# Kernel optimization log

Measured on AMD Instinct MI355X. Metric: run time of the kernel, lower is better.

## Reference

```python
import jax, jax.numpy as jnp
import numpy as np
from math import sqrt

IN_DIM = 4096
OUT_DIM = 32
TW = 2            # tree_width (forced to 2 by the forward's pairwise stacking)
TREE_DEPTH = 22
T = TREE_DEPTH - 1  # number of loop iterations (module decrements tree_depth)


def _w(k, out_dim, in_dim):
    # mimics init_weights_unif: U(-1,1)/sqrt(out_dim) + eye (preserve=True default)
    x = (jax.random.uniform(k, (out_dim, in_dim)) * 2 - 1) / sqrt(out_dim)
    return x + jnp.eye(out_dim, in_dim)


def _b(k, dim):
    return (jax.random.uniform(k, (dim,)) * 2 - 1) / sqrt(dim)


def setup_inputs() -> dict:
    key = jax.random.key(0)
    ks = jax.random.split(key, 14)
    return {
        "x": jax.random.normal(ks[0], (IN_DIM,), dtype=jnp.float32),
        "in_left_layer": _w(ks[1], TW, IN_DIM),
        "in_right_layer": _w(ks[2], TW, IN_DIM),
        "in_left_bias": _b(ks[3], TW),
        "in_right_bias": _b(ks[4], TW),
        "tree_left_layers": jnp.stack([_w(k, TW, TW) for k in jax.random.split(ks[5], T)]),
        "tree_right_layers": jnp.stack([_w(k, TW, TW) for k in jax.random.split(ks[6], T)]),
        "tree_left_biases": jnp.stack([_b(k, TW) for k in jax.random.split(ks[7], T)]),
        "tree_right_biases": jnp.stack([_b(k, TW) for k in jax.random.split(ks[8], T)]),
        "out_layer0": _w(ks[9], OUT_DIM, IN_DIM),
        "out_layers": jnp.stack([_w(k, OUT_DIM, TW) for k in jax.random.split(ks[10], T)]),
        "out_bias": _b(ks[11], OUT_DIM),
    }


def reference(x, in_left_layer, in_right_layer, in_left_bias, in_right_bias,
              tree_left_layers, tree_right_layers, tree_left_biases,
              tree_right_biases, out_layer0, out_layers, out_bias):
    # Faithful to BinTreeNetwork.forward: the per-j torch.tensor([li_j, ri_j])
    # construction is exactly jnp.stack([left, right], axis=1); the
    # ComponentNetwork is constructed in __init__ but never used in forward.
    left = x @ in_left_layer.T + in_left_bias      # (TW,)
    right = x @ in_right_layer.T + in_right_bias   # (TW,)
    out = x @ out_layer0.T                          # (OUT_DIM,)
    n_iter = tree_left_layers.shape[0]
    for i in range(n_iter):  # fixed small structural loop; shapes differ per level
        # res: binary-tree expansion, shape (2,)*(i+2); res[j,0]=left[j], res[j,1]=right[j]
        res = jnp.stack([left, right], axis=1)
        left = res @ tree_left_layers[i].T + tree_left_biases[i]
        right = res @ tree_right_layers[i].T + tree_right_biases[i]
        # out broadcasts: (2,)*i+(OUT_DIM,) + (2,)*(i+1)+(OUT_DIM,)
        out = out + res @ out_layers[i].T
    return out + out_bias  # shape (2,)*T + (OUT_DIM,)
```

## Files before the change

kernel.cpp:

```cpp
#include <hip/hip_runtime.h>
#include <hip/hip_bf16.h>


#define P0 (1u << 19)
#define C14OFF (1u << 20)
#define C16OFF (1u << 21)

typedef float floatx4 __attribute__((ext_vector_type(4)));

__global__ __launch_bounds__(1024) void k_dots(
    const float* __restrict__ x,
    const float* __restrict__ inL,
    const float* __restrict__ inR,
    const float* __restrict__ outL0,
    float* __restrict__ ws)
{
    __shared__ float red[16];
    const int d = blockIdx.x;
    const int tid = threadIdx.x;
    const float* row =
        (d < 2) ? inL + d * 4096 :
        (d < 4) ? inR + (d - 2) * 4096 :
                  outL0 + (d - 4) * 4096;
    floatx4 a = ((const floatx4*)row)[tid];
    floatx4 b = ((const floatx4*)x)[tid];
    float s = a.x * b.x + a.y * b.y + a.z * b.z + a.w * b.w;
    #pragma unroll
    for (int off = 32; off; off >>= 1) s += __shfl_down(s, off, 64);
    if ((tid & 63) == 0) red[tid >> 6] = s;
    __syncthreads();
    if (tid < 16) {
        float v = red[tid];
        #pragma unroll
        for (int off = 8; off; off >>= 1) v += __shfl_down(v, off, 16);
        if (tid == 0) ws[P0 + 1664 + d] = v;
    }
}

__global__ __launch_bounds__(256) void k_paths(
    const float* __restrict__ treeL,
    const float* __restrict__ treeR,
    const float* __restrict__ treeLb,
    const float* __restrict__ treeRb,
    const float* __restrict__ inLb,
    const float* __restrict__ inRb,
    float* __restrict__ ws)
{
    const unsigned t = blockIdx.x * 256u + threadIdx.x;
    const float* dots = ws + P0 + 1664;

    if (t < 2) {
        ws[t * 2 + 0] = dots[t]     + inLb[t];
        ws[t * 2 + 1] = dots[2 + t] + inRb[t];
    }
    if (t >= (1u << 18) - 4) return;

    const unsigned u = t + 4u;
    const int i = (31 - __clz(u)) - 1;
    unsigned m = u - (1u << (i + 1));
    unsigned sbits = 0;
    for (int l = i; l >= 1; --l) {
        sbits |= ((m >> (l - 1)) & 1u) << l;
        m = ((m >> l) << (l - 1)) | (m & ((1u << (l - 1)) - 1u));
    }
    float v0 = dots[m]     + inLb[m];
    float v1 = dots[2 + m] + inRb[m];
    for (int l = 1; l <= i; ++l) {
        const int s = (sbits >> l) & 1;
        const float* W  = (s ? treeR  : treeL)  + (l - 1) * 4;
        const float* bb = (s ? treeRb : treeLb) + (l - 1) * 2;
        const float n0 = W[0] * v0 + W[1] * v1 + bb[0];
        const float n1 = W[2] * v0 + W[3] * v1 + bb[1];
        v0 = n0; v1 = n1;
    }
    ws[2 * t + 4] = v0;
    ws[2 * t + 5] = v1;
}

__global__ __launch_bounds__(256) void k_c16f(
    const float* __restrict__ outLs,
    const float* __restrict__ outB,
    float* __restrict__ ws)
{
    const unsigned m = blockIdx.x * 256u + threadIdx.x;
    const float* dots = ws + P0 + 1664;

    float acc[32];
    #pragma unroll
    for (int o = 0; o < 32; ++o) acc[o] = dots[4 + o] + outB[o];
    #pragma unroll
    for (int i = 0; i <= 16; ++i) {
        const float2 v = *(const float2*)(ws + ((1u << (i + 2)) - 4)
                                             + (m & ((2u << i) - 1)) * 2);
        const float* cf = outLs + i * 64;
        #pragma unroll
        for (int o = 0; o < 32; ++o)
            acc[o] += v.x * cf[o * 2] + v.y * cf[o * 2 + 1];
    }
    floatx4* dst = (floatx4*)(ws + C16OFF + (size_t)m * 32);
    #pragma unroll
    for (int q = 0; q < 8; ++q)
        dst[q] = (floatx4){acc[q * 4 + 0], acc[q * 4 + 1],
                           acc[q * 4 + 2], acc[q * 4 + 3]};
}

__global__ __launch_bounds__(256) void k_final_c16(
    const float* __restrict__ ws,
    const float* __restrict__ outLs,
    const float* __restrict__ treeL,
    const float* __restrict__ treeR,
    const float* __restrict__ treeLb,
    const float* __restrict__ treeRb,
    float* __restrict__ out)
{
    __shared__ floatx4 st[256 * 8];
    const int tid = threadIdx.x;
    const unsigned B = blockIdx.x * 256u + tid;
    const float* C16 = ws + C16OFF;

    float acc[32];
    {
        const floatx4* c4 = (const floatx4*)(C16 + (size_t)(B & 0x1FFFFu) * 32);
        #pragma unroll
        for (int q = 0; q < 8; ++q) {
            floatx4 v = c4[q];
            acc[q * 4 + 0] = v.x; acc[q * 4 + 1] = v.y;
            acc[q * 4 + 2] = v.z; acc[q * 4 + 3] = v.w;
        }
    }

    {
        const unsigned Blo = B & 0xFFFFu;
        const float* r16 = ws + ((1u << 18) - 4);
        float2 vA = *(const float2*)(r16 + Blo * 2);
        float2 vC = *(const float2*)(r16 + (Blo + 65536u) * 2);
        float A0 = vA.x, A1 = vA.y;
        float c0 = vC.x, c1 = vC.y;
        #pragma unroll
        for (int l = 17; l <= 20; ++l) {
            const int s = (B >> (l - 1)) & 1;
            const float* WL = treeL  + (l - 1) * 4;
            const float* WR = treeR  + (l - 1) * 4;
            const float* bL = treeLb + (l - 1) * 2;
            const float* bR = treeRb + (l - 1) * 2;
            const float w00 = s ? WR[0] : WL[0], w01 = s ? WR[1] : WL[1];
            const float w10 = s ? WR[2] : WL[2], w11 = s ? WR[3] : WL[3];
            const float b0  = s ? bR[0] : bL[0], b1  = s ? bR[1] : bL[1];
            const float nA0 = w00 * A0 + w01 * A1 + b0;
            const float nA1 = w10 * A0 + w11 * A1 + b1;
            const float nc0 = w00 * c0 + w01 * c1 + b0;
            const float nc1 = w10 * c0 + w11 * c1 + b1;
            A0 = nA0; A1 = nA1; c0 = nc0; c1 = nc1;
            const int pick = (B >> l) & 1;
            const float q0 = pick ? c0 : A0, q1 = pick ? c1 : A1;
            const float* cf = outLs + l * 64;
            #pragma unroll
            for (int o = 0; o < 32; ++o)
                acc[o] += q0 * cf[o * 2] + q1 * cf[o * 2 + 1];
        }
    }

    #pragma unroll
    for (int q = 0; q < 8; ++q) {
        st[tid * 8 + (q ^ (tid & 7))] =
            (floatx4){acc[q * 4 + 0], acc[q * 4 + 1],
                      acc[q * 4 + 2], acc[q * 4 + 3]};
    }
    __syncthreads();
    {
        const int w = tid >> 6, lane = tid & 63;
        const int x = (lane & 7) ^ (lane >> 3);
        floatx4* dst = (floatx4*)(out + (size_t)blockIdx.x * 8192u
                                      + (unsigned)w * 2048u + (unsigned)lane * 4u);
        #pragma unroll
        for (int j = 0; j < 8; ++j) {
            const int m = w * 64 + j * 8 + (lane >> 3);
            __builtin_nontemporal_store(st[m * 8 + x], dst + j * 64);
        }
    }
}

__global__ __launch_bounds__(1024) void k_levels(
    const float* __restrict__ inLb,
    const float* __restrict__ inRb,
    const float* __restrict__ treeL,
    const float* __restrict__ treeR,
    const float* __restrict__ treeLb,
    const float* __restrict__ treeRb,
    const float* __restrict__ outLs,
    const float* __restrict__ outB,
    float* __restrict__ ws)
{
    const int tid = threadIdx.x;
    float* base  = ws + P0;
    float* outLf = ws + P0 + 32;
    float* tLf   = ws + P0 + 1376;
    float* tRf   = ws + P0 + 1460;
    float* tLbf  = ws + P0 + 1544;
    float* tRbf  = ws + P0 + 1586;
    const float* dots = ws + P0 + 1664;
    float* C7    = ws + P0 + 2048;

    for (int i = tid; i < 21 * 64; i += 1024) outLf[i] = outLs[i];
    if (tid < 84)                      tLf[tid]        = treeL[tid];
    else if (tid < 168)                tRf[tid - 84]   = treeR[tid - 84];
    else if (tid < 210)                tLbf[tid - 168] = treeLb[tid - 168];
    else if (tid < 252)                tRbf[tid - 210] = treeRb[tid - 210];
    if (tid < 32) base[tid] = dots[4 + tid] + outB[tid];
    if (tid < 2) {
        ws[tid * 2 + 0] = dots[tid]     + inLb[tid];
        ws[tid * 2 + 1] = dots[2 + tid] + inRb[tid];
    }
    __syncthreads();

    for (int i = 1; i <= 13; ++i) {
        const float* prev = ws + ((1u << (i + 1)) - 4);
        float* cur        = ws + ((1u << (i + 2)) - 4);
        const int rows = 1 << (i + 1);
        const int lowmask = (1 << (i - 1)) - 1;
        for (int m = tid; m < rows; m += 1024) {
            const int src = ((m >> i) << (i - 1)) | (m & lowmask);
            const int s = (m >> (i - 1)) & 1;
            const float* W  = (s ? tRf  : tLf)  + (i - 1) * 4;
            const float* bb = (s ? tRbf : tLbf) + (i - 1) * 2;
            const float p0 = prev[src * 2], p1 = prev[src * 2 + 1];
            cur[m * 2 + 0] = W[0] * p0 + W[1] * p1 + bb[0];
            cur[m * 2 + 1] = W[2] * p0 + W[3] * p1 + bb[1];
        }
        __syncthreads();
    }

    for (int idx = tid; idx < 8192; idx += 1024) {
        const int m = idx >> 5, o = idx & 31;
        float s = base[o];
        #pragma unroll
        for (int i = 0; i < 8; ++i) {
            const float* ri = ws + ((1u << (i + 2)) - 4) + (m & ((2 << i) - 1)) * 2;
            s += ri[0] * outLf[i * 64 + o * 2] + ri[1] * outLf[i * 64 + o * 2 + 1];
        }
        C7[idx] = s;
    }
}

__global__ __launch_bounds__(256) void k_mid(float* __restrict__ ws)
{
    const int blk = blockIdx.x;
    int j, b;
    if      (blk < 16) { j = 14; b = blk; }
    else if (blk < 48) { j = 15; b = blk - 16; }
    else               { j = 16; b = blk - 48; }

    const float* tLf  = ws + P0 + 1376;
    const float* tRf  = ws + P0 + 1460;
    const float* tLbf = ws + P0 + 1544;
    const float* tRbf = ws + P0 + 1586;

    unsigned m = (unsigned)b << 11;
    const unsigned basej = m;
    unsigned sbits = 0;
    for (int l = j; l > 13; --l) {
        sbits |= ((m >> (l - 1)) & 1u) << l;
        m = ((m >> l) << (l - 1)) | (m & ((1u << (l - 1)) - 1));
    }

    const int r0 = threadIdx.x * 8;
    const floatx4* s4 = (const floatx4*)(ws + ((1u << 15) - 4) + (m + r0) * 2);
    floatx4 a0 = s4[0], a1 = s4[1], a2 = s4[2], a3 = s4[3];
    float r[8][2] = {{a0.x,a0.y},{a0.z,a0.w},{a1.x,a1.y},{a1.z,a1.w},
                     {a2.x,a2.y},{a2.z,a2.w},{a3.x,a3.y},{a3.z,a3.w}};

    for (int l = 14; l <= j; ++l) {
        const int s = (sbits >> l) & 1;
        const float* W  = (s ? tRf  : tLf)  + (l - 1) * 4;
        const float* bb = (s ? tRbf : tLbf) + (l - 1) * 2;
        const float w00 = W[0], w01 = W[1], w10 = W[2], w11 = W[3];
        const float b0 = bb[0], b1 = bb[1];
        #pragma unroll
        for (int q = 0; q < 8; ++q) {
            const float p0 = r[q][0], p1 = r[q][1];
            r[q][0] = w00 * p0 + w01 * p1 + b0;
            r[q][1] = w10 * p0 + w11 * p1 + b1;
        }
    }

    floatx4* d4 = (floatx4*)(ws + ((1u << (j + 2)) - 4) + (basej + r0) * 2);
    d4[0] = (floatx4){r[0][0], r[0][1], r[1][0], r[1][1]};
    d4[1] = (floatx4){r[2][0], r[2][1], r[3][0], r[3][1]};
    d4[2] = (floatx4){r[4][0], r[4][1], r[5][0], r[5][1]};
    d4[3] = (floatx4){r[6][0], r[6][1], r[7][0], r[7][1]};
}

__global__ __launch_bounds__(256) void k_c14(float* __restrict__ ws)
{
    const unsigned m = blockIdx.x * 256u + threadIdx.x;
    const float* outLf = ws + P0 + 32;
    const float* C7    = ws + P0 + 2048;

    float acc[32];
    const floatx4* c4 = (const floatx4*)(C7 + (m & 255u) * 32);
    #pragma unroll
    for (int q = 0; q < 8; ++q) {
        floatx4 v = c4[q];
        acc[q * 4 + 0] = v.x; acc[q * 4 + 1] = v.y;
        acc[q * 4 + 2] = v.z; acc[q * 4 + 3] = v.w;
    }
    #pragma unroll
    for (int i = 8; i <= 14; ++i) {
        const float2 v = *(const float2*)(ws + ((1u << (i + 2)) - 4)
                                             + (m & ((2u << i) - 1)) * 2);
        const float* cf = outLf + i * 64;
        #pragma unroll
        for (int o = 0; o < 32; ++o)
            acc[o] += v.x * cf[o * 2] + v.y * cf[o * 2 + 1];
    }
    floatx4* dst = (floatx4*)(ws + C14OFF + m * 32);
    #pragma unroll
    for (int q = 0; q < 8; ++q)
        dst[q] = (floatx4){acc[q * 4 + 0], acc[q * 4 + 1],
                           acc[q * 4 + 2], acc[q * 4 + 3]};
}

__global__ __launch_bounds__(256) void k_final_fold(const float* __restrict__ ws,
                                                    float* __restrict__ out)
{
    __shared__ floatx4 st[256 * 8];
    const int tid = threadIdx.x;
    const unsigned B = blockIdx.x * 256u + tid;
    const float* outLf = ws + P0 + 32;
    const float* tLf   = ws + P0 + 1376;
    const float* tRf   = ws + P0 + 1460;
    const float* tLbf  = ws + P0 + 1544;
    const float* tRbf  = ws + P0 + 1586;
    const float* C14   = ws + C14OFF;

    float acc[32];
    {
        const floatx4* c4 = (const floatx4*)(C14 + (B & 0x7FFFu) * 32);
        #pragma unroll
        for (int q = 0; q < 8; ++q) {
            floatx4 v = c4[q];
            acc[q * 4 + 0] = v.x; acc[q * 4 + 1] = v.y;
            acc[q * 4 + 2] = v.z; acc[q * 4 + 3] = v.w;
        }
    }
    {
        const float2 v = *(const float2*)(ws + ((1u << 17) - 4)
                                             + (B & 0xFFFFu) * 2);
        const float* cf = outLf + 15 * 64;
        #pragma unroll
        for (int o = 0; o < 32; ++o)
            acc[o] += v.x * cf[o * 2] + v.y * cf[o * 2 + 1];
    }
    {
        const unsigned Blo = B & 0xFFFFu;
        const float* r16 = ws + ((1u << 18) - 4);
        float2 vA = *(const float2*)(r16 + Blo * 2);
        float2 vC = *(const float2*)(r16 + (Blo + 65536u) * 2);
        float A0 = vA.x, A1 = vA.y;
        float c0 = vC.x, c1 = vC.y;
        {
            const int pick = (B >> 16) & 1;
            const float q0 = pick ? c0 : A0, q1 = pick ? c1 : A1;
            const float* cf = outLf + 16 * 64;
            #pragma unroll
            for (int o = 0; o < 32; ++o)
                acc[o] += q0 * cf[o * 2] + q1 * cf[o * 2 + 1];
        }
        #pragma unroll
        for (int l = 17; l <= 20; ++l) {
            const int s = (B >> (l - 1)) & 1;
            const float* WL = tLf + (l - 1) * 4;
            const float* WR = tRf + (l - 1) * 4;
            const float* bL = tLbf + (l - 1) * 2;
            const float* bR = tRbf + (l - 1) * 2;
            const float w00 = s ? WR[0] : WL[0], w01 = s ? WR[1] : WL[1];
            const float w10 = s ? WR[2] : WL[2], w11 = s ? WR[3] : WL[3];
            const float b0  = s ? bR[0] : bL[0], b1  = s ? bR[1] : bL[1];
            const float nA0 = w00 * A0 + w01 * A1 + b0;
            const float nA1 = w10 * A0 + w11 * A1 + b1;
            const float nc0 = w00 * c0 + w01 * c1 + b0;
            const float nc1 = w10 * c0 + w11 * c1 + b1;
            A0 = nA0; A1 = nA1; c0 = nc0; c1 = nc1;
            const int pick = (B >> l) & 1;
            const float q0 = pick ? c0 : A0, q1 = pick ? c1 : A1;
            const float* cf = outLf + l * 64;
            #pragma unroll
            for (int o = 0; o < 32; ++o)
                acc[o] += q0 * cf[o * 2] + q1 * cf[o * 2 + 1];
        }
    }
    #pragma unroll
    for (int q = 0; q < 8; ++q) {
        st[tid * 8 + (q ^ (tid & 7))] =
            (floatx4){acc[q * 4 + 0], acc[q * 4 + 1],
                      acc[q * 4 + 2], acc[q * 4 + 3]};
    }
    __syncthreads();
    {
        const int w = tid >> 6, lane = tid & 63;
        const int x = (lane & 7) ^ (lane >> 3);
        floatx4* dst = (floatx4*)(out + (size_t)blockIdx.x * 8192u
                                      + (unsigned)w * 2048u + (unsigned)lane * 4u);
        #pragma unroll
        for (int j = 0; j < 8; ++j) {
            const int m = w * 64 + j * 8 + (lane >> 3);
            __builtin_nontemporal_store(st[m * 8 + x], dst + j * 64);
        }
    }
}

__global__ __launch_bounds__(256) void k_final_legacy(const float* __restrict__ ws,
                                                      float* __restrict__ out)
{
    __shared__ floatx4 st[256 * 8];
    const int tid = threadIdx.x;
    const unsigned B = blockIdx.x * 256u + tid;
    const float* outLf = ws + P0 + 32;
    const float* tLf   = ws + P0 + 1376;
    const float* tRf   = ws + P0 + 1460;
    const float* tLbf  = ws + P0 + 1544;
    const float* tRbf  = ws + P0 + 1586;
    const float* C7    = ws + P0 + 2048;

    float acc[32];
    {
        const floatx4* c4 = (const floatx4*)(C7 + (B & 255u) * 32);
        #pragma unroll
        for (int q = 0; q < 8; ++q) {
            floatx4 v = c4[q];
            acc[q * 4 + 0] = v.x; acc[q * 4 + 1] = v.y;
            acc[q * 4 + 2] = v.z; acc[q * 4 + 3] = v.w;
        }
    }
    float p[8][2];
    #pragma unroll
    for (int i = 8; i <= 15; ++i) {
        const float2* ri = (const float2*)(ws + ((1u << (i + 2)) - 4)
                                              + (B & ((2u << i) - 1)) * 2);
        float2 v = *ri;
        p[i - 8][0] = v.x;
        p[i - 8][1] = v.y;
    }
    #pragma unroll
    for (int i = 0; i < 8; ++i) {
        const float* cf = outLf + (i + 8) * 64;
        const float q0 = p[i][0], q1 = p[i][1];
        #pragma unroll
        for (int o = 0; o < 32; ++o)
            acc[o] += q0 * cf[o * 2] + q1 * cf[o * 2 + 1];
    }
    {
        const unsigned Blo = B & 0xFFFFu;
        const float* r16 = ws + ((1u << 18) - 4);
        float2 vA = *(const float2*)(r16 + Blo * 2);
        float2 vC = *(const float2*)(r16 + (Blo + 65536u) * 2);
        float A0 = vA.x, A1 = vA.y;
        float c0 = vC.x, c1 = vC.y;
        {
            const int pick = (B >> 16) & 1;
            const float q0 = pick ? c0 : A0, q1 = pick ? c1 : A1;
            const float* cf = outLf + 16 * 64;
            #pragma unroll
            for (int o = 0; o < 32; ++o)
                acc[o] += q0 * cf[o * 2] + q1 * cf[o * 2 + 1];
        }
        #pragma unroll
        for (int l = 17; l <= 20; ++l) {
            const int s = (B >> (l - 1)) & 1;
            const float* WL = tLf + (l - 1) * 4;
            const float* WR = tRf + (l - 1) * 4;
            const float* bL = tLbf + (l - 1) * 2;
            const float* bR = tRbf + (l - 1) * 2;
            const float w00 = s ? WR[0] : WL[0], w01 = s ? WR[1] : WL[1];
            const float w10 = s ? WR[2] : WL[2], w11 = s ? WR[3] : WL[3];
            const float b0  = s ? bR[0] : bL[0], b1  = s ? bR[1] : bL[1];
            const float nA0 = w00 * A0 + w01 * A1 + b0;
            const float nA1 = w10 * A0 + w11 * A1 + b1;
            const float nc0 = w00 * c0 + w01 * c1 + b0;
            const float nc1 = w10 * c0 + w11 * c1 + b1;
            A0 = nA0; A1 = nA1; c0 = nc0; c1 = nc1;
            const int pick = (B >> l) & 1;
            const float q0 = pick ? c0 : A0, q1 = pick ? c1 : A1;
            const float* cf = outLf + l * 64;
            #pragma unroll
            for (int o = 0; o < 32; ++o)
                acc[o] += q0 * cf[o * 2] + q1 * cf[o * 2 + 1];
        }
    }
    #pragma unroll
    for (int q = 0; q < 8; ++q) {
        st[tid * 8 + (q ^ (tid & 7))] =
            (floatx4){acc[q * 4 + 0], acc[q * 4 + 1],
                      acc[q * 4 + 2], acc[q * 4 + 3]};
    }
    __syncthreads();
    {
        const int w = tid >> 6, lane = tid & 63;
        const int x = (lane & 7) ^ (lane >> 3);
        floatx4* dst = (floatx4*)(out + (size_t)blockIdx.x * 8192u
                                      + (unsigned)w * 2048u + (unsigned)lane * 4u);
        #pragma unroll
        for (int j = 0; j < 8; ++j) {
            const int m = w * 64 + j * 8 + (lane >> 3);
            __builtin_nontemporal_store(st[m * 8 + x], dst + j * 64);
        }
    }
}

extern "C" void kernel_launch(void* const* d_in, const int* in_sizes, int n_in,
                              void* d_out, int out_size, void* d_ws, size_t ws_size,
                              hipStream_t stream) {
    const float* x     = (const float*)d_in[0];
    const float* inL   = (const float*)d_in[1];
    const float* inR   = (const float*)d_in[2];
    const float* inLb  = (const float*)d_in[3];
    const float* inRb  = (const float*)d_in[4];
    const float* treeL = (const float*)d_in[5];
    const float* treeR = (const float*)d_in[6];
    const float* treeLb= (const float*)d_in[7];
    const float* treeRb= (const float*)d_in[8];
    const float* outL0 = (const float*)d_in[9];
    const float* outLs = (const float*)d_in[10];
    const float* outB  = (const float*)d_in[11];
    float* ws = (float*)d_ws;
    float* out = (float*)d_out;

    const bool use_c16 = ws_size >= ((size_t)C16OFF + (1u << 22)) * sizeof(float);
    const bool use_c14 = ws_size >= ((size_t)C14OFF + (1u << 20)) * sizeof(float);

    hipLaunchKernelGGL(k_dots, dim3(36), dim3(1024), 0, stream,
                       x, inL, inR, outL0, ws);
    if (use_c16) {
        hipLaunchKernelGGL(k_paths, dim3(1024), dim3(256), 0, stream,
                           treeL, treeR, treeLb, treeRb, inLb, inRb, ws);
        hipLaunchKernelGGL(k_c16f, dim3(512), dim3(256), 0, stream,
                           outLs, outB, ws);
        hipLaunchKernelGGL(k_final_c16, dim3(1u << 13), dim3(256), 0, stream,
                           ws, outLs, treeL, treeR, treeLb, treeRb, out);
    } else {
        hipLaunchKernelGGL(k_levels, dim3(1), dim3(1024), 0, stream,
                           inLb, inRb, treeL, treeR, treeLb, treeRb, outLs, outB, ws);
        hipLaunchKernelGGL(k_mid, dim3(112), dim3(256), 0, stream, ws);
        if (use_c14) {
            hipLaunchKernelGGL(k_c14, dim3(128), dim3(256), 0, stream, ws);
            hipLaunchKernelGGL(k_final_fold, dim3(1u << 13), dim3(256), 0, stream, ws, out);
        } else {
            hipLaunchKernelGGL(k_final_legacy, dim3(1u << 13), dim3(256), 0, stream, ws, out);
        }
    }
}
```

Baseline: 334.7 us.

## Fuse tree-path evaluation into c16 accumulation kernel, dropping k_paths launch

Removes the separate k_paths kernel. The c16 accumulation kernel now recomputes each level's tree-path values in registers instead of reading them from the workspace. Only the level-16 path values are still written to the workspace, for the final kernel to use. This saves one launch and a workspace round trip, but adds redundant per-thread arithmetic and stops writing the other levels' values, which the final kernel must not rely on.

```diff
diff --git a/kernel.cpp b/kernel.cpp
--- a/kernel.cpp
+++ b/kernel.cpp
@@ -37,47 +37,13 @@
     }
 }
 
-__global__ __launch_bounds__(256) void k_paths(
+__global__ __launch_bounds__(256) void k_c16x(
     const float* __restrict__ treeL,
     const float* __restrict__ treeR,
     const float* __restrict__ treeLb,
     const float* __restrict__ treeRb,
     const float* __restrict__ inLb,
     const float* __restrict__ inRb,
-    float* __restrict__ ws)
-{
-    const unsigned t = blockIdx.x * 256u + threadIdx.x;
-    const float* dots = ws + P0 + 1664;
-
-    if (t < 2) {
-        ws[t * 2 + 0] = dots[t]     + inLb[t];
-        ws[t * 2 + 1] = dots[2 + t] + inRb[t];
-    }
-    if (t >= (1u << 18) - 4) return;
-
-    const unsigned u = t + 4u;
-    const int i = (31 - __clz(u)) - 1;
-    unsigned m = u - (1u << (i + 1));
-    unsigned sbits = 0;
-    for (int l = i; l >= 1; --l) {
-        sbits |= ((m >> (l - 1)) & 1u) << l;
-        m = ((m >> l) << (l - 1)) | (m & ((1u << (l - 1)) - 1u));
-    }
-    float v0 = dots[m]     + inLb[m];
-    float v1 = dots[2 + m] + inRb[m];
-    for (int l = 1; l <= i; ++l) {
-        const int s = (sbits >> l) & 1;
-        const float* W  = (s ? treeR  : treeL)  + (l - 1) * 4;
-        const float* bb = (s ? treeRb : treeLb) + (l - 1) * 2;
-        const float n0 = W[0] * v0 + W[1] * v1 + bb[0];
-        const float n1 = W[2] * v0 + W[3] * v1 + bb[1];
-        v0 = n0; v1 = n1;
-    }
-    ws[2 * t + 4] = v0;
-    ws[2 * t + 5] = v1;
-}
-
-__global__ __launch_bounds__(256) void k_c16f(
     const float* __restrict__ outLs,
     const float* __restrict__ outB,
     float* __restrict__ ws)
@@ -88,15 +54,44 @@
     float acc[32];
     #pragma unroll
     for (int o = 0; o < 32; ++o) acc[o] = dots[4 + o] + outB[o];
+
+    float v16_0 = 0.f, v16_1 = 0.f;
     #pragma unroll
     for (int i = 0; i <= 16; ++i) {
-        const float2 v = *(const float2*)(ws + ((1u << (i + 2)) - 4)
-                                             + (m & ((2u << i) - 1)) * 2);
+        unsigned mm = m & ((2u << i) - 1u);
+        unsigned sbits = 0;
+        #pragma unroll
+        for (int l = 16; l >= 1; --l) {
+            if (l <= i) {
+                sbits |= ((mm >> (l - 1)) & 1u) << l;
+                mm = ((mm >> l) << (l - 1)) | (mm & ((1u << (l - 1)) - 1u));
+            }
+        }
+        float v0 = dots[mm]     + inLb[mm];
+        float v1 = dots[2 + mm] + inRb[mm];
+        #pragma unroll
+        for (int l = 1; l <= 16; ++l) {
+            if (l <= i) {
+                const int s = (sbits >> l) & 1;
+                const float* W  = (s ? treeR  : treeL)  + (l - 1) * 4;
+                const float* bb = (s ? treeRb : treeLb) + (l - 1) * 2;
+                const float n0 = W[0] * v0 + W[1] * v1 + bb[0];
+                const float n1 = W[2] * v0 + W[3] * v1 + bb[1];
+                v0 = n0; v1 = n1;
+            }
+        }
         const float* cf = outLs + i * 64;
         #pragma unroll
         for (int o = 0; o < 32; ++o)
-            acc[o] += v.x * cf[o * 2] + v.y * cf[o * 2 + 1];
-    }
+            acc[o] += v0 * cf[o * 2] + v1 * cf[o * 2 + 1];
+        if (i == 16) { v16_0 = v0; v16_1 = v1; }
+    }
+
+    {
+        float2 t; t.x = v16_0; t.y = v16_1;
+        ((float2*)(ws + ((1u << 18) - 4)))[m] = t;
+    }
+
     floatx4* dst = (floatx4*)(ws + C16OFF + (size_t)m * 32);
     #pragma unroll
     for (int q = 0; q < 8; ++q)
@@ -531,9 +526,8 @@
     hipLaunchKernelGGL(k_dots, dim3(36), dim3(1024), 0, stream,
                        x, inL, inR, outL0, ws);
     if (use_c16) {
-        hipLaunchKernelGGL(k_paths, dim3(1024), dim3(256), 0, stream,
-                           treeL, treeR, treeLb, treeRb, inLb, inRb, ws);
-        hipLaunchKernelGGL(k_c16f, dim3(512), dim3(256), 0, stream,
+        hipLaunchKernelGGL(k_c16x, dim3(512), dim3(256), 0, stream,
+                           treeL, treeR, treeLb, treeRb, inLb, inRb,
                            outLs, outB, ws);
         hipLaunchKernelGGL(k_final_c16, dim3(1u << 13), dim3(256), 0, stream,
                            ws, outLs, treeL, treeR, treeLb, treeRb, out);
```

Measured after the change: 336.7 us. Within noise of the previous version (+0.6%).
